# Kernel optimization log

Measured on AMD Instinct MI355X. Metric: run time of the kernel, lower is better.

## Reference

```python
import jax, jax.numpy as jnp
import numpy as np

FIELD_DIMS = [50000, 5000, 2000, 1000, 1000, 500, 300, 200]
OFFSETS = np.concatenate([[0], np.cumsum(FIELD_DIMS)[:-1]]).astype(np.int64)
INPUT_DIM = int(np.sum(FIELD_DIMS))  # 60000
NUM_FIELDS = len(FIELD_DIMS)         # 8
EMBED_DIM = 16
MLP_DIMS = [256, 128, 64]
BATCH = 2048


def _xavier(key, shape):
    fan_in, fan_out = shape[0], shape[1]
    bound = float(np.sqrt(6.0 / (fan_in + fan_out)))
    return jax.random.uniform(key, shape, jnp.float32, -bound, bound)


def setup_inputs() -> dict:
    key = jax.random.key(0)
    ks = jax.random.split(key, 16)
    # per-field indices in valid range
    cols = [jax.random.randint(jax.random.fold_in(ks[0], f), (BATCH,), 0, FIELD_DIMS[f], dtype=jnp.int64)
            for f in range(NUM_FIELDS)]
    x = jnp.stack(cols, axis=1)  # [B, F] int64
    emb_table = _xavier(ks[1], (INPUT_DIM, EMBED_DIM))  # concat of per-field nn.Embedding tables
    # FM linear: torch init uniform_(weight) in [0,1), zero bias
    w_lin = jax.random.uniform(ks[2], (INPUT_DIM,), jnp.float32)
    b_lin = jnp.zeros((), jnp.float32)
    dnn_in = NUM_FIELDS * EMBED_DIM  # 128
    w1 = _xavier(ks[3], (dnn_in, MLP_DIMS[0]));  b1 = jnp.zeros((MLP_DIMS[0],), jnp.float32)
    w2 = _xavier(ks[4], (MLP_DIMS[0], MLP_DIMS[1])); b2 = jnp.zeros((MLP_DIMS[1],), jnp.float32)
    w3 = _xavier(ks[5], (MLP_DIMS[1], MLP_DIMS[2])); b3 = jnp.zeros((MLP_DIMS[2],), jnp.float32)
    w_last = _xavier(ks[6], (MLP_DIMS[2], 1))  # no bias
    return {"x": x, "emb_table": emb_table, "w_lin": w_lin, "b_lin": b_lin,
            "w1": w1, "b1": b1, "w2": w2, "b2": b2, "w3": w3, "b3": b3, "w_last": w_last}


def reference(x, emb_table, w_lin, b_lin, w1, b1, w2, b2, w3, b3, w_last):
    B = x.shape[0]
    offsets = jnp.asarray(OFFSETS)
    x_off = x + offsets[None, :]                        # [B, F] global feature ids
    # embedding gathers (equivalent to per-field nn.Embedding on one concat table)
    dense_x = emb_table[x_off]                          # [B, F, D]
    # one-hot scatter + dense linear (faithful to original memory pattern)
    sparse_x = jnp.zeros((B, INPUT_DIM), jnp.float32).at[
        jnp.arange(B)[:, None], x_off].set(1.0)        # [B, input_dim]
    linear_out = sparse_x @ w_lin + b_lin               # [B]
    # FM second-order pooling
    square_of_sum = jnp.sum(dense_x, axis=1) ** 2       # [B, D]
    sum_of_square = jnp.sum(dense_x ** 2, axis=1)       # [B, D]
    fm_out = 0.5 * jnp.sum(square_of_sum - sum_of_square, axis=1)  # [B]
    y_fm = linear_out + fm_out
    # DNN component (dropout=0, no BN)
    h = dense_x.reshape(B, -1)                          # [B, F*D]
    h = jax.nn.relu(h @ w1 + b1)
    h = jax.nn.relu(h @ w2 + b2)
    h = jax.nn.relu(h @ w3 + b3)
    y_dnn = (h @ w_last)[:, 0]                          # [B]
    return y_fm + y_dnn
```

## Files before the change

kernel.cpp:

```cpp
#include <hip/hip_runtime.h>


#define NF   8
#define ED   16
#define IN0  128
#define N1   256
#define N2   128
#define N3   64
#define EPB  4
#define T    512

__device__ const int g_off[NF] = {0, 50000, 55000, 57000, 58000, 59000, 59500, 59800};

__global__ __launch_bounds__(T, 4) void deepfm_fused(
    const int*   __restrict__ x,
    const float* __restrict__ emb,
    const float* __restrict__ wlin,
    const float* __restrict__ blin,
    const float* __restrict__ w1,
    const float* __restrict__ b1,
    const float* __restrict__ w2,
    const float* __restrict__ b2,
    const float* __restrict__ w3,
    const float* __restrict__ b3,
    const float* __restrict__ wlast,
    float*       __restrict__ out)
{
    __shared__ float h0[EPB][IN0];
    __shared__ float h1[EPB][N1];
    __shared__ float h2[EPB][N2];
    __shared__ float ps[7 * EPB * N2];
    __shared__ float base[EPB];

    const int tid = threadIdx.x;
    const int b0  = blockIdx.x * EPB;

    {
        const int r = tid >> 7;
        const int f = (tid >> 4) & 7;
        const int d = tid & 15;
        const int idx = x[(b0 + r) * NF + f] + g_off[f];
        h0[r][f * ED + d] = emb[idx * ED + d];
    }

    if (tid < 32) {
        const int r = tid >> 3, f = tid & 7;
        float lin = wlin[x[(b0 + r) * NF + f] + g_off[f]];
        lin += __shfl_xor(lin, 1);
        lin += __shfl_xor(lin, 2);
        lin += __shfl_xor(lin, 4);
        if (f == 0) base[r] = lin + blin[0];
    }
    __syncthreads();

    if (tid < 64) {
        const int r = tid >> 4, d = tid & 15;
        float s = 0.0f, ss = 0.0f;
        #pragma unroll
        for (int f = 0; f < NF; ++f) {
            const float v = h0[r][f * ED + d];
            s += v;
            ss = fmaf(v, v, ss);
        }
        float p = 0.5f * (s * s - ss);
        p += __shfl_xor(p, 1);
        p += __shfl_xor(p, 2);
        p += __shfl_xor(p, 4);
        p += __shfl_xor(p, 8);
        if (d == 0) base[r] += p;
    }

    {
        const int c2    = (tid & 127) * 2;
        const int seg   = tid >> 7;
        const int kbase = seg * 32;
        float2 acc[EPB];
        const float2 bb = (seg == 0) ? *(const float2*)(b1 + c2) : make_float2(0.f, 0.f);
        #pragma unroll
        for (int e = 0; e < EPB; ++e) acc[e] = bb;

        #pragma unroll 2
        for (int k0 = 0; k0 < 32; k0 += 4) {
            float4 hv[EPB];
            #pragma unroll
            for (int e = 0; e < EPB; ++e) hv[e] = *(const float4*)(&h0[e][kbase + k0]);
            #pragma unroll
            for (int i = 0; i < 4; ++i) {
                const float2 w = *(const float2*)(w1 + (kbase + k0 + i) * N1 + c2);
                #pragma unroll
                for (int e = 0; e < EPB; ++e) {
                    const float hk = (i == 0) ? hv[e].x : (i == 1) ? hv[e].y
                                   : (i == 2) ? hv[e].z : hv[e].w;
                    acc[e].x = fmaf(hk, w.x, acc[e].x);
                    acc[e].y = fmaf(hk, w.y, acc[e].y);
                }
            }
        }
        if (seg != 0) {
            #pragma unroll
            for (int e = 0; e < EPB; ++e)
                *(float2*)(&ps[(seg - 1) * (EPB * N1) + e * N1 + c2]) = acc[e];
        }
        __syncthreads();
        if (seg == 0) {
            #pragma unroll
            for (int e = 0; e < EPB; ++e) {
                float2 v = acc[e];
                #pragma unroll
                for (int s = 0; s < 3; ++s) {
                    const float2 q = *(const float2*)(&ps[s * (EPB * N1) + e * N1 + c2]);
                    v.x += q.x; v.y += q.y;
                }
                h1[e][c2]     = fmaxf(v.x, 0.0f);
                h1[e][c2 + 1] = fmaxf(v.y, 0.0f);
            }
        }
    }
    __syncthreads();

    {
        const int c2    = (tid & 63) * 2;
        const int seg   = tid >> 6;
        const int kbase = seg * 32;
        float2 acc[EPB];
        #pragma unroll
        for (int e = 0; e < EPB; ++e) acc[e] = make_float2(0.f, 0.f);

        #pragma unroll 2
        for (int k0 = 0; k0 < 32; k0 += 4) {
            float4 hv[EPB];
            #pragma unroll
            for (int e = 0; e < EPB; ++e) hv[e] = *(const float4*)(&h1[e][kbase + k0]);
            #pragma unroll
            for (int i = 0; i < 4; ++i) {
                const float2 w = *(const float2*)(w2 + (kbase + k0 + i) * N2 + c2);
                #pragma unroll
                for (int e = 0; e < EPB; ++e) {
                    const float hk = (i == 0) ? hv[e].x : (i == 1) ? hv[e].y
                                   : (i == 2) ? hv[e].z : hv[e].w;
                    acc[e].x = fmaf(hk, w.x, acc[e].x);
                    acc[e].y = fmaf(hk, w.y, acc[e].y);
                }
            }
        }
        if (seg != 0) {
            #pragma unroll
            for (int e = 0; e < EPB; ++e)
                *(float2*)(&ps[(seg - 1) * (EPB * N2) + e * N2 + c2]) = acc[e];
        }
        __syncthreads();
        if (seg == 0) {
            const float2 bb = *(const float2*)(b2 + c2);
            #pragma unroll
            for (int e = 0; e < EPB; ++e) {
                float2 v = acc[e];
                #pragma unroll
                for (int s = 0; s < 7; ++s) {
                    const float2 q = *(const float2*)(&ps[s * (EPB * N2) + e * N2 + c2]);
                    v.x += q.x; v.y += q.y;
                }
                h2[e][c2]     = fmaxf(v.x + bb.x, 0.0f);
                h2[e][c2 + 1] = fmaxf(v.y + bb.y, 0.0f);
            }
        }
    }
    __syncthreads();

    {
        const int c     = tid & 63;
        const int seg   = tid >> 6;
        const int kbase = seg * 16;
        float acc[EPB];
        #pragma unroll
        for (int e = 0; e < EPB; ++e) acc[e] = 0.0f;

        #pragma unroll
        for (int k0 = 0; k0 < 16; k0 += 4) {
            float4 hv[EPB];
            #pragma unroll
            for (int e = 0; e < EPB; ++e) hv[e] = *(const float4*)(&h2[e][kbase + k0]);
            #pragma unroll
            for (int i = 0; i < 4; ++i) {
                const float w = w3[(kbase + k0 + i) * N3 + c];
                #pragma unroll
                for (int e = 0; e < EPB; ++e) {
                    const float hk = (i == 0) ? hv[e].x : (i == 1) ? hv[e].y
                                   : (i == 2) ? hv[e].z : hv[e].w;
                    acc[e] = fmaf(hk, w, acc[e]);
                }
            }
        }
        if (seg != 0) {
            #pragma unroll
            for (int e = 0; e < EPB; ++e)
                ps[(seg - 1) * (EPB * N3) + e * N3 + c] = acc[e];
        }
        __syncthreads();

        if (tid < 64) {
            const float bb = b3[c];
            const float wl = wlast[c];
            float t[EPB];
            #pragma unroll
            for (int e = 0; e < EPB; ++e) {
                float v = acc[e] + bb;
                #pragma unroll
                for (int s = 0; s < 7; ++s) v += ps[s * (EPB * N3) + e * N3 + c];
                t[e] = fmaxf(v, 0.0f) * wl;
            }
            #pragma unroll
            for (int off = 1; off < 64; off <<= 1) {
                #pragma unroll
                for (int e = 0; e < EPB; ++e) t[e] += __shfl_xor(t[e], off);
            }
            if (tid == 0) {
                #pragma unroll
                for (int e = 0; e < EPB; ++e) out[b0 + e] = base[e] + t[e];
            }
        }
    }
}

extern "C" void kernel_launch(void* const* d_in, const int* in_sizes, int n_in,
                              void* d_out, int out_size, void* d_ws, size_t ws_size,
                              hipStream_t stream) {
    const int*   x     = (const int*)d_in[0];
    const float* emb   = (const float*)d_in[1];
    const float* wlin  = (const float*)d_in[2];
    const float* blin  = (const float*)d_in[3];
    const float* w1    = (const float*)d_in[4];
    const float* b1    = (const float*)d_in[5];
    const float* w2    = (const float*)d_in[6];
    const float* b2    = (const float*)d_in[7];
    const float* w3    = (const float*)d_in[8];
    const float* b3    = (const float*)d_in[9];
    const float* wlast = (const float*)d_in[10];
    float* out = (float*)d_out;

    const int batch = in_sizes[0] / NF;
    dim3 grid(batch / EPB);
    deepfm_fused<<<grid, T, 0, stream>>>(x, emb, wlin, blin,
                                         w1, b1, w2, b2, w3, b3, wlast, out);
}
```

Baseline: 16.58 us.

## Double rows per block to 1024 threads and parallelize split-K reductions

Raises the block to 8 batch rows and 1024 threads, which halves the grid to 256 blocks. Every thread now writes its split-K partial sums to shared memory, and a separate pass spreads the reduction across all rows and columns instead of leaving it to one segment. The aim is more reuse of each weight load across rows and a shorter serial reduction tail. In exchange it needs more shared memory (about 64KB for the partial-sum buffer), may allow fewer resident blocks per CU under __launch_bounds__(1024,4), and leaves fewer blocks than CUs to spread the work.

```diff
diff --git a/kernel.cpp b/kernel.cpp
--- a/kernel.cpp
+++ b/kernel.cpp
@@ -7,8 +7,8 @@
 #define N1   256
 #define N2   128
 #define N3   64
-#define EPB  4
-#define T    512
+#define EPB  8
+#define T    1024
 
 __device__ const int g_off[NF] = {0, 50000, 55000, 57000, 58000, 59000, 59500, 59800};
 
@@ -29,7 +29,7 @@
     __shared__ float h0[EPB][IN0];
     __shared__ float h1[EPB][N1];
     __shared__ float h2[EPB][N2];
-    __shared__ float ps[7 * EPB * N2];
+    __shared__ float ps[16 * EPB * N2];
     __shared__ float base[EPB];
 
     const int tid = threadIdx.x;
@@ -43,7 +43,7 @@
         h0[r][f * ED + d] = emb[idx * ED + d];
     }
 
-    if (tid < 32) {
+    if (tid < 64) {
         const int r = tid >> 3, f = tid & 7;
         float lin = wlin[x[(b0 + r) * NF + f] + g_off[f]];
         lin += __shfl_xor(lin, 1);
@@ -53,7 +53,7 @@
     }
     __syncthreads();
 
-    if (tid < 64) {
+    if (tid < 128) {
         const int r = tid >> 4, d = tid & 15;
         float s = 0.0f, ss = 0.0f;
         #pragma unroll
@@ -71,22 +71,21 @@
     }
 
     {
-        const int c2    = (tid & 127) * 2;
-        const int seg   = tid >> 7;
-        const int kbase = seg * 32;
+        const int c2 = (tid & 127) * 2;
+        const int sg = tid >> 7;
+        const int kb = sg * 16;
         float2 acc[EPB];
-        const float2 bb = (seg == 0) ? *(const float2*)(b1 + c2) : make_float2(0.f, 0.f);
-        #pragma unroll
-        for (int e = 0; e < EPB; ++e) acc[e] = bb;
-
-        #pragma unroll 2
-        for (int k0 = 0; k0 < 32; k0 += 4) {
+        #pragma unroll
+        for (int e = 0; e < EPB; ++e) acc[e] = make_float2(0.f, 0.f);
+
+        #pragma unroll
+        for (int k0 = 0; k0 < 16; k0 += 4) {
             float4 hv[EPB];
             #pragma unroll
-            for (int e = 0; e < EPB; ++e) hv[e] = *(const float4*)(&h0[e][kbase + k0]);
+            for (int e = 0; e < EPB; ++e) hv[e] = *(const float4*)(&h0[e][kb + k0]);
             #pragma unroll
             for (int i = 0; i < 4; ++i) {
-                const float2 w = *(const float2*)(w1 + (kbase + k0 + i) * N1 + c2);
+                const float2 w = *(const float2*)(w1 + (kb + k0 + i) * N1 + c2);
                 #pragma unroll
                 for (int e = 0; e < EPB; ++e) {
                     const float hk = (i == 0) ? hv[e].x : (i == 1) ? hv[e].y
@@ -96,44 +95,42 @@
                 }
             }
         }
-        if (seg != 0) {
-            #pragma unroll
-            for (int e = 0; e < EPB; ++e)
-                *(float2*)(&ps[(seg - 1) * (EPB * N1) + e * N1 + c2]) = acc[e];
-        }
-        __syncthreads();
-        if (seg == 0) {
-            #pragma unroll
-            for (int e = 0; e < EPB; ++e) {
-                float2 v = acc[e];
-                #pragma unroll
-                for (int s = 0; s < 3; ++s) {
-                    const float2 q = *(const float2*)(&ps[s * (EPB * N1) + e * N1 + c2]);
-                    v.x += q.x; v.y += q.y;
-                }
-                h1[e][c2]     = fmaxf(v.x, 0.0f);
-                h1[e][c2 + 1] = fmaxf(v.y, 0.0f);
-            }
-        }
-    }
-    __syncthreads();
-
-    {
-        const int c2    = (tid & 63) * 2;
-        const int seg   = tid >> 6;
-        const int kbase = seg * 32;
+        #pragma unroll
+        for (int e = 0; e < EPB; ++e)
+            *(float2*)(&ps[(sg * EPB + e) * N1 + c2]) = acc[e];
+    }
+    __syncthreads();
+
+    {
+        const int r  = tid >> 7;
+        const int c2 = (tid & 127) * 2;
+        float2 v = *(const float2*)(b1 + c2);
+        #pragma unroll
+        for (int s = 0; s < 8; ++s) {
+            const float2 q = *(const float2*)(&ps[(s * EPB + r) * N1 + c2]);
+            v.x += q.x; v.y += q.y;
+        }
+        h1[r][c2]     = fmaxf(v.x, 0.0f);
+        h1[r][c2 + 1] = fmaxf(v.y, 0.0f);
+    }
+    __syncthreads();
+
+    {
+        const int c2 = (tid & 63) * 2;
+        const int sg = tid >> 6;
+        const int kb = sg * 16;
         float2 acc[EPB];
         #pragma unroll
         for (int e = 0; e < EPB; ++e) acc[e] = make_float2(0.f, 0.f);
 
-        #pragma unroll 2
-        for (int k0 = 0; k0 < 32; k0 += 4) {
+        #pragma unroll
+        for (int k0 = 0; k0 < 16; k0 += 4) {
             float4 hv[EPB];
             #pragma unroll
-            for (int e = 0; e < EPB; ++e) hv[e] = *(const float4*)(&h1[e][kbase + k0]);
+            for (int e = 0; e < EPB; ++e) hv[e] = *(const float4*)(&h1[e][kb + k0]);
             #pragma unroll
             for (int i = 0; i < 4; ++i) {
-                const float2 w = *(const float2*)(w2 + (kbase + k0 + i) * N2 + c2);
+                const float2 w = *(const float2*)(w2 + (kb + k0 + i) * N2 + c2);
                 #pragma unroll
                 for (int e = 0; e < EPB; ++e) {
                     const float hk = (i == 0) ? hv[e].x : (i == 1) ? hv[e].y
@@ -143,45 +140,38 @@
                 }
             }
         }
-        if (seg != 0) {
-            #pragma unroll
-            for (int e = 0; e < EPB; ++e)
-                *(float2*)(&ps[(seg - 1) * (EPB * N2) + e * N2 + c2]) = acc[e];
-        }
-        __syncthreads();
-        if (seg == 0) {
-            const float2 bb = *(const float2*)(b2 + c2);
-            #pragma unroll
-            for (int e = 0; e < EPB; ++e) {
-                float2 v = acc[e];
-                #pragma unroll
-                for (int s = 0; s < 7; ++s) {
-                    const float2 q = *(const float2*)(&ps[s * (EPB * N2) + e * N2 + c2]);
-                    v.x += q.x; v.y += q.y;
-                }
-                h2[e][c2]     = fmaxf(v.x + bb.x, 0.0f);
-                h2[e][c2 + 1] = fmaxf(v.y + bb.y, 0.0f);
-            }
-        }
-    }
-    __syncthreads();
-
-    {
-        const int c     = tid & 63;
-        const int seg   = tid >> 6;
-        const int kbase = seg * 16;
+        #pragma unroll
+        for (int e = 0; e < EPB; ++e)
+            *(float2*)(&ps[(sg * EPB + e) * N2 + c2]) = acc[e];
+    }
+    __syncthreads();
+
+    {
+        const int r = tid >> 7;
+        const int c = tid & 127;
+        float v = b2[c];
+        #pragma unroll
+        for (int s = 0; s < 16; ++s) v += ps[(s * EPB + r) * N2 + c];
+        h2[r][c] = fmaxf(v, 0.0f);
+    }
+    __syncthreads();
+
+    {
+        const int c  = tid & 63;
+        const int sg = tid >> 6;
+        const int kb = sg * 8;
         float acc[EPB];
         #pragma unroll
         for (int e = 0; e < EPB; ++e) acc[e] = 0.0f;
 
         #pragma unroll
-        for (int k0 = 0; k0 < 16; k0 += 4) {
+        for (int k0 = 0; k0 < 8; k0 += 4) {
             float4 hv[EPB];
             #pragma unroll
-            for (int e = 0; e < EPB; ++e) hv[e] = *(const float4*)(&h2[e][kbase + k0]);
+            for (int e = 0; e < EPB; ++e) hv[e] = *(const float4*)(&h2[e][kb + k0]);
             #pragma unroll
             for (int i = 0; i < 4; ++i) {
-                const float w = w3[(kbase + k0 + i) * N3 + c];
+                const float w = w3[(kb + k0 + i) * N3 + c];
                 #pragma unroll
                 for (int e = 0; e < EPB; ++e) {
                     const float hk = (i == 0) ? hv[e].x : (i == 1) ? hv[e].y
@@ -190,34 +180,22 @@
                 }
             }
         }
-        if (seg != 0) {
-            #pragma unroll
-            for (int e = 0; e < EPB; ++e)
-                ps[(seg - 1) * (EPB * N3) + e * N3 + c] = acc[e];
-        }
-        __syncthreads();
-
-        if (tid < 64) {
-            const float bb = b3[c];
-            const float wl = wlast[c];
-            float t[EPB];
-            #pragma unroll
-            for (int e = 0; e < EPB; ++e) {
-                float v = acc[e] + bb;
-                #pragma unroll
-                for (int s = 0; s < 7; ++s) v += ps[s * (EPB * N3) + e * N3 + c];
-                t[e] = fmaxf(v, 0.0f) * wl;
-            }
-            #pragma unroll
-            for (int off = 1; off < 64; off <<= 1) {
-                #pragma unroll
-                for (int e = 0; e < EPB; ++e) t[e] += __shfl_xor(t[e], off);
-            }
-            if (tid == 0) {
-                #pragma unroll
-                for (int e = 0; e < EPB; ++e) out[b0 + e] = base[e] + t[e];
-            }
-        }
+        #pragma unroll
+        for (int e = 0; e < EPB; ++e)
+            ps[(sg * EPB + e) * N3 + c] = acc[e];
+    }
+    __syncthreads();
+
+    if (tid < 512) {
+        const int r = tid >> 6;
+        const int c = tid & 63;
+        float v = b3[c];
+        #pragma unroll
+        for (int s = 0; s < 16; ++s) v += ps[(s * EPB + r) * N3 + c];
+        float t = fmaxf(v, 0.0f) * wlast[c];
+        #pragma unroll
+        for (int off = 1; off < 64; off <<= 1) t += __shfl_xor(t, off);
+        if (c == 0) out[b0 + r] = base[r] + t;
     }
 }
 
```

Result: faster. 13.50 us (-18.5%).
